# Kernel optimization log

Measured on AMD Instinct MI355X. Metric: run time of the kernel, lower is better.

The kernel has to match this reference:

```python
import jax, jax.numpy as jnp
import numpy as np

B, S = 512, 64          # batch, grain grid size (coarse==medium==fine==64, see notes)
N = S * S               # tokens per image
CONTENT_PAD, CONTENT_EOS = 1024, 1025
COARSE_POS_PAD, COARSE_POS_EOS = 128, 129
MEDIUM_POS_PAD, MEDIUM_POS_EOS = 256, 257
FINE_POS_PAD, FINE_POS_EOS = 1024, 1025


def setup_inputs() -> dict:
    key = jax.random.key(0)
    k1, k2 = jax.random.split(key)
    indices = jax.random.randint(k1, (B, S, S), 0, 1024, dtype=jnp.int32)
    grain_indices = jax.random.randint(k2, (B, S, S), 0, 3, dtype=jnp.int32)
    return {"indices": indices, "grain_indices": grain_indices}


def _compact(vals, mask, eos, pad):
    """Stable stream-compaction per row: selected vals first, then EOS, then PAD.
    vals/mask: [B, N].  Output: [B, N+1] (static max length; torch pads to batch max)."""
    b, n = vals.shape
    # stable argsort of (not mask) brings True positions to the front, in order
    order = jnp.argsort(jnp.where(mask, 0, 1).astype(jnp.int32), axis=1, stable=True)
    sel = jnp.take_along_axis(vals, order, axis=1)                  # [B, N]
    sel = jnp.concatenate([sel, jnp.zeros((b, 1), vals.dtype)], axis=1)  # [B, N+1]
    cnt = jnp.sum(mask.astype(jnp.int32), axis=1, keepdims=True)    # [B, 1]
    slot = jnp.arange(n + 1, dtype=jnp.int32)[None, :]              # [1, N+1]
    out = jnp.where(slot < cnt, sel,
                    jnp.where(slot == cnt, jnp.asarray(eos, vals.dtype),
                              jnp.asarray(pad, vals.dtype)))
    return out


def reference(indices, grain_indices):
    b, s, _ = indices.shape
    n = s * s
    # With coarse==medium==fine the module's rearranges are identity reshapes:
    # coarse_content = medium_content source = fine_content source = flattened grid,
    # and all three position sequences are row-major arange(n).
    flat = indices.reshape(b, n)
    g = grain_indices.reshape(b, n)
    pos = jnp.broadcast_to(jnp.arange(n, dtype=indices.dtype), (b, n))

    coarse_content = _compact(flat, g == 0, CONTENT_EOS, CONTENT_PAD)
    coarse_position = _compact(pos, g == 0, COARSE_POS_EOS, COARSE_POS_PAD)
    medium_content = _compact(flat, g == 1, CONTENT_EOS, CONTENT_PAD)
    medium_position = _compact(pos, g == 1, MEDIUM_POS_EOS, MEDIUM_POS_PAD)
    fine_content = _compact(flat, g == 2, CONTENT_EOS, CONTENT_PAD)
    fine_position = _compact(pos, g == 2, FINE_POS_EOS, FINE_POS_PAD)

    coarse_segment = jnp.zeros_like(coarse_content)
    medium_segment = jnp.ones_like(medium_content)
    fine_segment = jnp.full_like(fine_content, 2)
    return (coarse_content, medium_content, fine_content,
            coarse_position, medium_position, fine_position,
            coarse_segment, medium_segment, fine_segment)
```

## Files before the change

kernel.cpp:

```cpp
#include <hip/hip_runtime.h>


constexpr int N_TOK  = 4096;
constexpr int M_OUT  = N_TOK + 1;
constexpr int TPB    = 1024;
constexpr int NWAVES = TPB / 64;
constexpr int EPT    = N_TOK / TPB;

constexpr int CONTENT_PAD = 1024, CONTENT_EOS = 1025;
__device__ __constant__ int POS_PAD[3] = {128, 256, 1024};
__device__ __constant__ int POS_EOS[3] = {129, 257, 1025};

__global__ __launch_bounds__(TPB, 8) void
triple_grain_permute(const int* __restrict__ indices,
                     const int* __restrict__ grain,
                     int* __restrict__ out,
                     int batch) {
    const int b = blockIdx.x;
    const int t = threadIdx.x;
    const int lane = t & 63;
    const int wave = t >> 6;

    const int* idx_row = indices + (size_t)b * N_TOK;
    const int* g_row   = grain   + (size_t)b * N_TOK;

    __shared__ int s_packed[N_TOK];
    __shared__ unsigned long long s_wave_tot[NWAVES];

    int4 gg = reinterpret_cast<const int4*>(g_row)[t];
    int4 ii = reinterpret_cast<const int4*>(idx_row)[t];
    int gv[EPT] = {gg.x, gg.y, gg.z, gg.w};
    const int elem0 = t * EPT;
    int pv[EPT] = {ii.x | (elem0 << 12),
                   ii.y | ((elem0 + 1) << 12),
                   ii.z | ((elem0 + 2) << 12),
                   ii.w | ((elem0 + 3) << 12)};

    int c0 = 0, c1 = 0, c2 = 0;
#pragma unroll
    for (int j = 0; j < EPT; ++j) {
        c0 += (gv[j] == 0);
        c1 += (gv[j] == 1);
        c2 += (gv[j] == 2);
    }
    unsigned long long packed =
        (unsigned long long)c0 |
        ((unsigned long long)c1 << 21) |
        ((unsigned long long)c2 << 42);

    unsigned long long inc = packed;
#pragma unroll
    for (int off = 1; off < 64; off <<= 1) {
        unsigned long long nb =
            (unsigned long long)__shfl_up((long long)inc, off, 64);
        if (lane >= off) inc += nb;
    }
    if (lane == 63) s_wave_tot[wave] = inc;
    __syncthreads();

    unsigned long long wave_prefix = 0, total = 0;
#pragma unroll
    for (int w = 0; w < NWAVES; ++w) {
        unsigned long long v = s_wave_tot[w];
        if (w < wave) wave_prefix += v;
        total += v;
    }
    const unsigned long long excl = wave_prefix + (inc - packed);

    const int o0 = (int)(excl & 0x1FFFFF);
    const int o1 = (int)((excl >> 21) & 0x1FFFFF);
    const int o2 = (int)((excl >> 42) & 0x1FFFFF);
    const int cnt0 = (int)(total & 0x1FFFFF);
    const int cnt1 = (int)((total >> 21) & 0x1FFFFF);
    const int cnt2 = (int)((total >> 42) & 0x1FFFFF);

    const int base0 = 0, base1 = cnt0, base2 = cnt0 + cnt1;

    int d0 = base0 + o0, d1 = base1 + o1, d2 = base2 + o2;
#pragma unroll
    for (int j = 0; j < EPT; ++j) {
        const int c = gv[j];
        const int dst = (c == 0) ? d0 : ((c == 1) ? d1 : d2);
        s_packed[dst] = pv[j];
        d0 += (c == 0);
        d1 += (c == 1);
        d2 += (c == 2);
    }
    __syncthreads();

    const size_t ARR = (size_t)batch * M_OUT;
    const int bases[3] = {base0, base1, base2};
    const int cnts[3]  = {cnt0, cnt1, cnt2};

#pragma unroll
    for (int c = 0; c < 3; ++c) {
        int* dst_c = out + (size_t)c       * ARR + (size_t)b * M_OUT;
        int* dst_p = out + (size_t)(3 + c) * ARR + (size_t)b * M_OUT;
        int* dst_s = out + (size_t)(6 + c) * ARR + (size_t)b * M_OUT;
        const int cnt = cnts[c];
        const int base = bases[c];
        const int peos = POS_EOS[c], ppad = POS_PAD[c];
        for (int slot = t; slot < M_OUT; slot += TPB) {
            int vc, vp;
            if (slot < cnt) {
                const int p = s_packed[base + slot];
                vc = p & 0xFFF;
                vp = p >> 12;
            } else if (slot == cnt) {
                vc = CONTENT_EOS;
                vp = peos;
            } else {
                vc = CONTENT_PAD;
                vp = ppad;
            }
            dst_c[slot] = vc;
            dst_p[slot] = vp;
            dst_s[slot] = c;
        }
    }
}

extern "C" void kernel_launch(void* const* d_in, const int* in_sizes, int n_in,
                              void* d_out, int out_size, void* d_ws, size_t ws_size,
                              hipStream_t stream) {
    const int* indices = (const int*)d_in[0];
    const int* grain   = (const int*)d_in[1];
    int* out = (int*)d_out;

    const int batch = in_sizes[0] / N_TOK;
    triple_grain_permute<<<batch, TPB, 0, stream>>>(indices, grain, out, batch);
}
```

Before: 91.00 us.

## Vectorize output stores with aligned int4 chunks and 32-bit packed scan

Output rows of length 4097 are written with 16-byte int4 stores after peeling a few scalar elements to reach alignment that depends on the batch index, plus a scalar tail. The per-row scan now packs the three class counts into 10-bit fields of a 32-bit word instead of 21-bit fields of a 64-bit word, so each shuffle moves 32 bits. Shared-memory reads are clamped so slots past the valid range stay in bounds. The 10-bit fields suffice for per-wave counts (at most 256), and the full-row totals are summed in separate integers.

```diff
diff --git a/kernel.cpp b/kernel.cpp
--- a/kernel.cpp
+++ b/kernel.cpp
@@ -25,7 +25,7 @@
     const int* g_row   = grain   + (size_t)b * N_TOK;
 
     __shared__ int s_packed[N_TOK];
-    __shared__ unsigned long long s_wave_tot[NWAVES];
+    __shared__ unsigned int s_wave_tot[NWAVES];
 
     int4 gg = reinterpret_cast<const int4*>(g_row)[t];
     int4 ii = reinterpret_cast<const int4*>(idx_row)[t];
@@ -43,36 +43,30 @@
         c1 += (gv[j] == 1);
         c2 += (gv[j] == 2);
     }
-    unsigned long long packed =
-        (unsigned long long)c0 |
-        ((unsigned long long)c1 << 21) |
-        ((unsigned long long)c2 << 42);
+    unsigned int packed = (unsigned)c0 | ((unsigned)c1 << 10) | ((unsigned)c2 << 20);
 
-    unsigned long long inc = packed;
+    unsigned int inc = packed;
 #pragma unroll
     for (int off = 1; off < 64; off <<= 1) {
-        unsigned long long nb =
-            (unsigned long long)__shfl_up((long long)inc, off, 64);
+        unsigned int nb = (unsigned int)__shfl_up((int)inc, off, 64);
         if (lane >= off) inc += nb;
     }
     if (lane == 63) s_wave_tot[wave] = inc;
     __syncthreads();
 
-    unsigned long long wave_prefix = 0, total = 0;
+    int wp0 = 0, wp1 = 0, wp2 = 0, tot0 = 0, tot1 = 0, tot2 = 0;
 #pragma unroll
     for (int w = 0; w < NWAVES; ++w) {
-        unsigned long long v = s_wave_tot[w];
-        if (w < wave) wave_prefix += v;
-        total += v;
+        const unsigned int v = s_wave_tot[w];
+        const int f0 = v & 1023, f1 = (v >> 10) & 1023, f2 = (v >> 20) & 1023;
+        if (w < wave) { wp0 += f0; wp1 += f1; wp2 += f2; }
+        tot0 += f0; tot1 += f1; tot2 += f2;
     }
-    const unsigned long long excl = wave_prefix + (inc - packed);
-
-    const int o0 = (int)(excl & 0x1FFFFF);
-    const int o1 = (int)((excl >> 21) & 0x1FFFFF);
-    const int o2 = (int)((excl >> 42) & 0x1FFFFF);
-    const int cnt0 = (int)(total & 0x1FFFFF);
-    const int cnt1 = (int)((total >> 21) & 0x1FFFFF);
-    const int cnt2 = (int)((total >> 42) & 0x1FFFFF);
+    const unsigned int exv = inc - packed;
+    const int o0 = wp0 + (int)(exv & 1023);
+    const int o1 = wp1 + (int)((exv >> 10) & 1023);
+    const int o2 = wp2 + (int)((exv >> 20) & 1023);
+    const int cnt0 = tot0, cnt1 = tot1, cnt2 = tot2;
 
     const int base0 = 0, base1 = cnt0, base2 = cnt0 + cnt1;
 
@@ -89,6 +83,10 @@
     __syncthreads();
 
     const size_t ARR = (size_t)batch * M_OUT;
+    const int peel = (4 - (b & 3)) & 3;
+    const int nch  = (M_OUT - peel) >> 2;
+    const int rem  = (M_OUT - peel) & 3;
+
     const int bases[3] = {base0, base1, base2};
     const int cnts[3]  = {cnt0, cnt1, cnt2};
 
@@ -100,22 +98,36 @@
         const int cnt = cnts[c];
         const int base = bases[c];
         const int peos = POS_EOS[c], ppad = POS_PAD[c];
-        for (int slot = t; slot < M_OUT; slot += TPB) {
+
+        auto elem = [&](int slot, int& vc, int& vp) {
+            int a = base + slot;
+            a = (a > N_TOK - 1) ? (N_TOK - 1) : a;
+            const int pk = s_packed[a];
+            vc = (slot < cnt) ? (pk & 0xFFF) : ((slot == cnt) ? CONTENT_EOS : CONTENT_PAD);
+            vp = (slot < cnt) ? (pk >> 12)   : ((slot == cnt) ? peos : ppad);
+        };
+
+        if (t < peel) {
             int vc, vp;
-            if (slot < cnt) {
-                const int p = s_packed[base + slot];
-                vc = p & 0xFFF;
-                vp = p >> 12;
-            } else if (slot == cnt) {
-                vc = CONTENT_EOS;
-                vp = peos;
-            } else {
-                vc = CONTENT_PAD;
-                vp = ppad;
-            }
-            dst_c[slot] = vc;
-            dst_p[slot] = vp;
-            dst_s[slot] = c;
+            elem(t, vc, vp);
+            dst_c[t] = vc; dst_p[t] = vp; dst_s[t] = c;
+        }
+        if (t < nch) {
+            const int s0 = peel + 4 * t;
+            int4 vc4, vp4;
+            elem(s0 + 0, vc4.x, vp4.x);
+            elem(s0 + 1, vc4.y, vp4.y);
+            elem(s0 + 2, vc4.z, vp4.z);
+            elem(s0 + 3, vc4.w, vp4.w);
+            *reinterpret_cast<int4*>(dst_c + s0) = vc4;
+            *reinterpret_cast<int4*>(dst_p + s0) = vp4;
+            *reinterpret_cast<int4*>(dst_s + s0) = make_int4(c, c, c, c);
+        }
+        if (t < rem) {
+            const int slot = M_OUT - rem + t;
+            int vc, vp;
+            elem(slot, vc, vp);
+            dst_c[slot] = vc; dst_p[slot] = vp; dst_s[slot] = c;
         }
     }
 }
```

New measurement: 90.92 us. Within noise of the previous version (-0.1%).
